# Performance work log

Hardware: AMD Instinct MI355X
Metric: run time of the kernel (lower is better)

Reference implementation:

```python
import jax, jax.numpy as jnp
import numpy as np


def setup_inputs() -> dict:
    key = jax.random.key(0)
    k_x, k_B, k_C, k_D, k_step = jax.random.split(key, 5)
    Bsz, L, H = 8, 4096, 512
    P = 256  # effective state dim = dim_ssm_state // 2 (conj_sym)
    # s4d_inv init for Lambda (complex, stored as real/imag parts)
    n = jnp.arange(P, dtype=jnp.float32)
    Lambda_re = -0.5 * jnp.ones((P,), dtype=jnp.float32)
    Lambda_im = (P / np.pi) * (P / (2.0 * n + 1.0) - 1.0)
    # lecun_normal-ish init for B (P,H,2) and C (H,P,2), divided by sqrt(2)
    B = jax.random.normal(k_B, (P, H, 2), dtype=jnp.float32) * (1.0 / np.sqrt(H)) / np.sqrt(2.0)
    C = jax.random.normal(k_C, (H, P, 2), dtype=jnp.float32) * (1.0 / np.sqrt(P)) / np.sqrt(2.0)
    D = jax.random.normal(k_D, (H,), dtype=jnp.float32)
    dt_min, dt_max = 1e-3, 1e-1
    log_step = jax.random.uniform(k_step, (P,)) * (np.log(dt_max) - np.log(dt_min)) + np.log(dt_min)
    x = jax.random.normal(k_x, (Bsz, L, H), dtype=jnp.float32)
    return {"x": x, "Lambda_re": Lambda_re, "Lambda_im": Lambda_im,
            "B": B, "C": C, "D": D, "log_step": log_step.astype(jnp.float32)}


def _binary_op(q_i, q_j):
    A_i, b_i = q_i
    A_j, b_j = q_j
    return (A_j * A_i, A_j * b_i + b_j)


def reference(x, Lambda_re, Lambda_im, B, C, D, log_step):
    # Assemble complex params (conj_sym=True)
    Lam = Lambda_re + 1j * Lambda_im          # (P,)
    B_tilde = B[..., 0] + 1j * B[..., 1]      # (P,H)
    C_tilde = C[..., 0] + 1j * C[..., 1]      # (H,P)
    step = jnp.exp(log_step)                  # (P,) step_rescale = 1.0
    # ZOH discretization
    Lambda_bar = jnp.exp(Lam * step)                              # (P,)
    B_bar = ((Lambda_bar - 1.0) / Lam)[:, None] * B_tilde         # (P,H)
    # Bu elements: (Bsz, L, P) complex
    Bu = jnp.einsum('blh,ph->blp', x.astype(B_bar.dtype), B_bar)
    Lam_elems = jnp.broadcast_to(Lambda_bar, Bu.shape)
    # Parallel linear recurrence over time axis
    _, xs = jax.lax.associative_scan(_binary_op, (Lam_elems, Bu), axis=1)
    # Output projection with conjugate symmetry + D skip
    ys = 2.0 * jnp.einsum('blp,hp->blh', xs, C_tilde).real + D * x
    return ys
```

## Files before the change

### kernel.cpp

```cpp
#include <hip/hip_runtime.h>
#include <hip/hip_bf16.h>
#include <hip/hip_fp16.h>
#include <math.h>

#define BSZ 8
#define LSEQ 4096
#define HDIM 512
#define PDIM 256
#define MROWS (BSZ * LSEQ)
#define NDIM 512
#define CHUNK 64
#define NCHUNK (LSEQ / CHUNK)

typedef __attribute__((ext_vector_type(8))) short bf16x8;
typedef __attribute__((ext_vector_type(4))) float f32x4;

__global__ __launch_bounds__(256) void convert_x(const float* __restrict__ x,
                                                 __hip_bfloat16* __restrict__ xb,
                                                 int n4) {
    int i = blockIdx.x * blockDim.x + threadIdx.x;
    if (i >= n4) return;
    float4 v = ((const float4*)x)[i];
    union { ushort4 u; __hip_bfloat16 h[4]; } o;
    o.h[0] = __float2bfloat16(v.x);
    o.h[1] = __float2bfloat16(v.y);
    o.h[2] = __float2bfloat16(v.z);
    o.h[3] = __float2bfloat16(v.w);
    ((ushort4*)xb)[i] = o.u;
}

__global__ void precompute_w1(const float* __restrict__ Lre,
                              const float* __restrict__ Lim,
                              const float* __restrict__ logstep,
                              const float* __restrict__ Bmat,
                              __hip_bfloat16* __restrict__ W1T,
                              float* __restrict__ a_re,
                              float* __restrict__ a_im) {
    int idx = blockIdx.x * blockDim.x + threadIdx.x;
    if (idx >= PDIM * HDIM) return;
    int p = idx / HDIM, h = idx % HDIM;
    double step = exp((double)logstep[p]);
    double dlr = (double)Lre[p], dli = (double)Lim[p];
    double mag = exp(dlr * step);
    double ar = mag * cos(dli * step);
    double ai = mag * sin(dli * step);
    double den = dlr * dlr + dli * dli;
    double nr = ar - 1.0, ni = ai;
    double fr = (nr * dlr + ni * dli) / den;
    double fi = (ni * dlr - nr * dli) / den;
    double br = (double)Bmat[(size_t)(p * HDIM + h) * 2 + 0];
    double bi = (double)Bmat[(size_t)(p * HDIM + h) * 2 + 1];
    W1T[(size_t)(2 * p) * HDIM + h]     = __float2bfloat16((float)(fr * br - fi * bi));
    W1T[(size_t)(2 * p + 1) * HDIM + h] = __float2bfloat16((float)(fr * bi + fi * br));
    if (h == 0) { a_re[p] = (float)ar; a_im[p] = (float)ai; }
}

__global__ void precompute_w2(const float* __restrict__ Cmat,
                              __hip_bfloat16* __restrict__ W2T) {
    int idx = blockIdx.x * blockDim.x + threadIdx.x;
    if (idx >= HDIM * PDIM) return;
    int h = idx / PDIM, p = idx % PDIM;
    float cr = Cmat[(size_t)(h * PDIM + p) * 2 + 0];
    float ci = Cmat[(size_t)(h * PDIM + p) * 2 + 1];
    W2T[(size_t)h * NDIM + 2 * p]     = __float2bfloat16(2.0f * cr);
    W2T[(size_t)h * NDIM + 2 * p + 1] = __float2bfloat16(-2.0f * ci);
}

template <typename OT, bool SKIP>
__global__ __launch_bounds__(256) void gemm_bt(
    const __hip_bfloat16* __restrict__ A,
    const __hip_bfloat16* __restrict__ BT,
    OT* __restrict__ C,
    const float* __restrict__ Dvec,
    const __hip_bfloat16* __restrict__ Xskip,
    int M, int N, int K) {
    __shared__ __hip_bfloat16 smA[128 * 32];
    __shared__ __hip_bfloat16 smB[128 * 32];

    const int tid = threadIdx.x;
    const int lane = tid & 63;
    const int wave = tid >> 6;
    const int row0 = blockIdx.x * 128;
    const int col0 = blockIdx.y * 128;
    const int wm = (wave >> 1) * 64;
    const int wn = (wave & 1) * 64;

    const int sr = lane >> 2;
    const int sk = (lane & 3) * 8;
    const int quad = lane >> 4;
    const int l15 = lane & 15;

    f32x4 acc[4][4] = {};

    for (int k0 = 0; k0 < K; k0 += 32) {
#pragma unroll
        for (int q = 0; q < 2; ++q) {
            const int chunk = wave * 32 + q * 16;
            const __hip_bfloat16* gA = A + (size_t)(row0 + chunk + sr) * K + k0 + sk;
            __builtin_amdgcn_global_load_lds(
                (const __attribute__((address_space(1))) void*)gA,
                (__attribute__((address_space(3))) void*)&smA[chunk * 32], 16, 0, 0);
            const __hip_bfloat16* gB = BT + (size_t)(col0 + chunk + sr) * K + k0 + sk;
            __builtin_amdgcn_global_load_lds(
                (const __attribute__((address_space(1))) void*)gB,
                (__attribute__((address_space(3))) void*)&smB[chunk * 32], 16, 0, 0);
        }
        __syncthreads();

        bf16x8 af[4], bfr[4];
#pragma unroll
        for (int i = 0; i < 4; ++i)
            af[i] = *(const bf16x8*)&smA[(wm + i * 16 + l15) * 32 + quad * 8];
#pragma unroll
        for (int j = 0; j < 4; ++j)
            bfr[j] = *(const bf16x8*)&smB[(wn + j * 16 + l15) * 32 + quad * 8];
#pragma unroll
        for (int i = 0; i < 4; ++i)
#pragma unroll
            for (int j = 0; j < 4; ++j)
                acc[i][j] = __builtin_amdgcn_mfma_f32_16x16x32_bf16(
                    af[i], bfr[j], acc[i][j], 0, 0, 0);
        __syncthreads();
    }

#pragma unroll
    for (int i = 0; i < 4; ++i) {
        const int mbase = row0 + wm + i * 16 + quad * 4;
#pragma unroll
        for (int j = 0; j < 4; ++j) {
            const int col = col0 + wn + j * 16 + l15;
            const float dv = SKIP ? Dvec[col] : 0.0f;
#pragma unroll
            for (int r = 0; r < 4; ++r) {
                const size_t m = (size_t)(mbase + r);
                float v = acc[i][j][r];
                if (SKIP) v += dv * __bfloat162float(Xskip[m * N + col]);
                if constexpr (sizeof(OT) == 2) {
                    C[m * N + col] = OT(v);
                } else {
                    C[m * N + col] = v;
                }
            }
        }
    }
}

__global__ __launch_bounds__(256) void scan_chunks(const __half2* __restrict__ Bu2,
                                                   const float* __restrict__ a_re,
                                                   const float* __restrict__ a_im,
                                                   float2* __restrict__ S) {
    int b = blockIdx.x / NCHUNK;
    int c = blockIdx.x % NCHUNK;
    int p = threadIdx.x;
    float ar = a_re[p], ai = a_im[p];
    float sr = 0.0f, si = 0.0f;
    size_t m0 = (size_t)b * LSEQ + (size_t)c * CHUNK;
    for (int j = 0; j < CHUNK; ++j) {
        float2 u = __half22float2(Bu2[(m0 + j) * PDIM + p]);
        float nsr = ar * sr - ai * si + u.x;
        float nsi = ar * si + ai * sr + u.y;
        sr = nsr; si = nsi;
    }
    S[(size_t)(b * NCHUNK + c) * PDIM + p] = make_float2(sr, si);
}

__global__ __launch_bounds__(256) void scan_carry(const float2* __restrict__ S,
                                                  const float* __restrict__ a_re,
                                                  const float* __restrict__ a_im,
                                                  float2* __restrict__ carry) {
    int b = blockIdx.x;
    int p = threadIdx.x;
    double ar = (double)a_re[p], ai = (double)a_im[p];
#pragma unroll
    for (int i = 0; i < 6; ++i) {
        double nr = ar * ar - ai * ai;
        double ni = 2.0 * ar * ai;
        ar = nr; ai = ni;
    }
    float alr = (float)ar, ali = (float)ai;
    float cr = 0.0f, ci = 0.0f;
    for (int c = 0; c < NCHUNK; ++c) {
        carry[(size_t)(b * NCHUNK + c) * PDIM + p] = make_float2(cr, ci);
        float2 s = S[(size_t)(b * NCHUNK + c) * PDIM + p];
        float ncr = alr * cr - ali * ci + s.x;
        float nci = alr * ci + ali * cr + s.y;
        cr = ncr; ci = nci;
    }
}

__global__ __launch_bounds__(256) void scan_apply(const __half2* __restrict__ Bu2,
                                                  const float* __restrict__ a_re,
                                                  const float* __restrict__ a_im,
                                                  const float2* __restrict__ carry,
                                                  ushort2* __restrict__ xsb2) {
    int b = blockIdx.x / NCHUNK;
    int c = blockIdx.x % NCHUNK;
    int p = threadIdx.x;
    float ar = a_re[p], ai = a_im[p];
    float2 c0 = carry[(size_t)(b * NCHUNK + c) * PDIM + p];
    float sr = c0.x, si = c0.y;
    size_t m0 = (size_t)b * LSEQ + (size_t)c * CHUNK;
    for (int j = 0; j < CHUNK; ++j) {
        size_t idx = (m0 + j) * PDIM + p;
        float2 u = __half22float2(Bu2[idx]);
        float nsr = ar * sr - ai * si + u.x;
        float nsi = ar * si + ai * sr + u.y;
        sr = nsr; si = nsi;
        union { ushort2 u2; __hip_bfloat16 h[2]; } o;
        o.h[0] = __float2bfloat16(sr);
        o.h[1] = __float2bfloat16(si);
        xsb2[idx] = o.u2;
    }
}

extern "C" void kernel_launch(void* const* d_in, const int* in_sizes, int n_in,
                              void* d_out, int out_size, void* d_ws, size_t ws_size,
                              hipStream_t stream) {
    const float* x       = (const float*)d_in[0];
    const float* Lre     = (const float*)d_in[1];
    const float* Lim     = (const float*)d_in[2];
    const float* Bmat    = (const float*)d_in[3];
    const float* Cmat    = (const float*)d_in[4];
    const float* Dvec    = (const float*)d_in[5];
    const float* logstep = (const float*)d_in[6];
    float* out = (float*)d_out;

    char* ws = (char*)d_ws;
    const size_t MB = 1u << 20;
    __hip_bfloat16* xb  = (__hip_bfloat16*)(ws + 0);
    __hip_bfloat16* xsb = (__hip_bfloat16*)(ws + 32 * MB);
    __half* Bu          = (__half*)(ws + 64 * MB);
    __hip_bfloat16* W1T = (__hip_bfloat16*)(ws + 96 * MB);
    __hip_bfloat16* W2T = (__hip_bfloat16*)(ws + 96 * MB + 512 * 1024);
    float*  a_re  = (float*)(ws + 97 * MB);
    float*  a_im  = (float*)(ws + 97 * MB + 4096);
    float2* S     = (float2*)(ws + 98 * MB);
    float2* carry = (float2*)(ws + 99 * MB);

    convert_x<<<(MROWS * HDIM / 4 + 255) / 256, 256, 0, stream>>>(
        x, xb, MROWS * HDIM / 4);
    precompute_w1<<<(PDIM * HDIM + 255) / 256, 256, 0, stream>>>(
        Lre, Lim, logstep, Bmat, W1T, a_re, a_im);
    precompute_w2<<<(HDIM * PDIM + 255) / 256, 256, 0, stream>>>(Cmat, W2T);

    dim3 ggrid(MROWS / 128, NDIM / 128);
    gemm_bt<__half, false><<<ggrid, 256, 0, stream>>>(
        xb, W1T, Bu, nullptr, nullptr, MROWS, NDIM, HDIM);

    scan_chunks<<<BSZ * NCHUNK, 256, 0, stream>>>((const __half2*)Bu, a_re, a_im, S);
    scan_carry<<<BSZ, 256, 0, stream>>>(S, a_re, a_im, carry);
    scan_apply<<<BSZ * NCHUNK, 256, 0, stream>>>((const __half2*)Bu, a_re, a_im,
                                                 carry, (ushort2*)xsb);

    dim3 ggrid2(MROWS / 128, HDIM / 128);
    gemm_bt<float, true><<<ggrid2, 256, 0, stream>>>(
        xsb, W2T, out, Dvec, xb, MROWS, HDIM, NDIM);
}
```

Baseline: 223.5 us.

## Double-buffer GEMM LDS, parallelize carry scan, hoist per-state discretization

The GEMM now keeps two LDS buffers and issues the next k-tile's global-to-LDS loads before computing the current tile, with one barrier per iteration, so load latency can overlap the MFMA work. The serial 64-step carry scan (8 blocks) becomes a wave-level Hillis-Steele shuffle scan across chunks, with one wave per (batch, state). The double-precision discretization, including the chunk-power of Lambda_bar, moves into a small one-block kernel so W1 construction runs in float instead of repeating the double math per element. These changes cost twice the LDS per GEMM block, which may lower occupancy, plus an extra kernel launch, and the shuffle scan may round slightly differently.

```diff
diff --git a/kernel.cpp b/kernel.cpp
--- a/kernel.cpp
+++ b/kernel.cpp
@@ -29,16 +29,14 @@
     ((ushort4*)xb)[i] = o.u;
 }
 
-__global__ void precompute_w1(const float* __restrict__ Lre,
-                              const float* __restrict__ Lim,
-                              const float* __restrict__ logstep,
-                              const float* __restrict__ Bmat,
-                              __hip_bfloat16* __restrict__ W1T,
-                              float* __restrict__ a_re,
-                              float* __restrict__ a_im) {
-    int idx = blockIdx.x * blockDim.x + threadIdx.x;
-    if (idx >= PDIM * HDIM) return;
-    int p = idx / HDIM, h = idx % HDIM;
+__global__ void precompute_params(const float* __restrict__ Lre,
+                                  const float* __restrict__ Lim,
+                                  const float* __restrict__ logstep,
+                                  float* __restrict__ f_re, float* __restrict__ f_im,
+                                  float* __restrict__ a_re, float* __restrict__ a_im,
+                                  float* __restrict__ al_re, float* __restrict__ al_im) {
+    int p = threadIdx.x;
+    if (p >= PDIM) return;
     double step = exp((double)logstep[p]);
     double dlr = (double)Lre[p], dli = (double)Lim[p];
     double mag = exp(dlr * step);
@@ -46,13 +44,33 @@
     double ai = mag * sin(dli * step);
     double den = dlr * dlr + dli * dli;
     double nr = ar - 1.0, ni = ai;
-    double fr = (nr * dlr + ni * dli) / den;
-    double fi = (ni * dlr - nr * dli) / den;
-    double br = (double)Bmat[(size_t)(p * HDIM + h) * 2 + 0];
-    double bi = (double)Bmat[(size_t)(p * HDIM + h) * 2 + 1];
-    W1T[(size_t)(2 * p) * HDIM + h]     = __float2bfloat16((float)(fr * br - fi * bi));
-    W1T[(size_t)(2 * p + 1) * HDIM + h] = __float2bfloat16((float)(fr * bi + fi * br));
-    if (h == 0) { a_re[p] = (float)ar; a_im[p] = (float)ai; }
+    f_re[p] = (float)((nr * dlr + ni * dli) / den);
+    f_im[p] = (float)((ni * dlr - nr * dli) / den);
+    a_re[p] = (float)ar;
+    a_im[p] = (float)ai;
+    double cr = ar, ci = ai;
+#pragma unroll
+    for (int i = 0; i < 6; ++i) {
+        double tr = cr * cr - ci * ci;
+        double ti = 2.0 * cr * ci;
+        cr = tr; ci = ti;
+    }
+    al_re[p] = (float)cr;
+    al_im[p] = (float)ci;
+}
+
+__global__ __launch_bounds__(256) void precompute_w1(
+    const float* __restrict__ f_re, const float* __restrict__ f_im,
+    const float* __restrict__ Bmat,
+    __hip_bfloat16* __restrict__ W1T) {
+    int idx = blockIdx.x * blockDim.x + threadIdx.x;
+    if (idx >= PDIM * HDIM) return;
+    int p = idx / HDIM, h = idx % HDIM;
+    float fr = f_re[p], fi = f_im[p];
+    float br = Bmat[(size_t)(p * HDIM + h) * 2 + 0];
+    float bi = Bmat[(size_t)(p * HDIM + h) * 2 + 1];
+    W1T[(size_t)(2 * p) * HDIM + h]     = __float2bfloat16(fr * br - fi * bi);
+    W1T[(size_t)(2 * p + 1) * HDIM + h] = __float2bfloat16(fr * bi + fi * br);
 }
 
 __global__ void precompute_w2(const float* __restrict__ Cmat,
@@ -74,8 +92,8 @@
     const float* __restrict__ Dvec,
     const __hip_bfloat16* __restrict__ Xskip,
     int M, int N, int K) {
-    __shared__ __hip_bfloat16 smA[128 * 32];
-    __shared__ __hip_bfloat16 smB[128 * 32];
+    __shared__ __hip_bfloat16 smA[2 * 128 * 32];
+    __shared__ __hip_bfloat16 smB[2 * 128 * 32];
 
     const int tid = threadIdx.x;
     const int lane = tid & 63;
@@ -92,35 +110,48 @@
 
     f32x4 acc[4][4] = {};
 
-    for (int k0 = 0; k0 < K; k0 += 32) {
+    auto stage = [&](int buf, int k0) {
 #pragma unroll
         for (int q = 0; q < 2; ++q) {
             const int chunk = wave * 32 + q * 16;
             const __hip_bfloat16* gA = A + (size_t)(row0 + chunk + sr) * K + k0 + sk;
             __builtin_amdgcn_global_load_lds(
                 (const __attribute__((address_space(1))) void*)gA,
-                (__attribute__((address_space(3))) void*)&smA[chunk * 32], 16, 0, 0);
+                (__attribute__((address_space(3))) void*)&smA[buf * 4096 + chunk * 32],
+                16, 0, 0);
             const __hip_bfloat16* gB = BT + (size_t)(col0 + chunk + sr) * K + k0 + sk;
             __builtin_amdgcn_global_load_lds(
                 (const __attribute__((address_space(1))) void*)gB,
-                (__attribute__((address_space(3))) void*)&smB[chunk * 32], 16, 0, 0);
+                (__attribute__((address_space(3))) void*)&smB[buf * 4096 + chunk * 32],
+                16, 0, 0);
         }
-        __syncthreads();
-
+    };
+
+    const int nk = K >> 5;
+    stage(0, 0);
+    __syncthreads();
+    int cur = 0;
+    for (int t = 0; t < nk; ++t) {
+        if (t + 1 < nk) stage(cur ^ 1, (t + 1) << 5);
+
+        const __hip_bfloat16* sA = &smA[cur * 4096];
+        const __hip_bfloat16* sB = &smB[cur * 4096];
         bf16x8 af[4], bfr[4];
 #pragma unroll
         for (int i = 0; i < 4; ++i)
-            af[i] = *(const bf16x8*)&smA[(wm + i * 16 + l15) * 32 + quad * 8];
+            af[i] = *(const bf16x8*)&sA[(wm + i * 16 + l15) * 32 + quad * 8];
 #pragma unroll
         for (int j = 0; j < 4; ++j)
-            bfr[j] = *(const bf16x8*)&smB[(wn + j * 16 + l15) * 32 + quad * 8];
+            bfr[j] = *(const bf16x8*)&sB[(wn + j * 16 + l15) * 32 + quad * 8];
 #pragma unroll
         for (int i = 0; i < 4; ++i)
 #pragma unroll
             for (int j = 0; j < 4; ++j)
                 acc[i][j] = __builtin_amdgcn_mfma_f32_16x16x32_bf16(
                     af[i], bfr[j], acc[i][j], 0, 0, 0);
+
         __syncthreads();
+        cur ^= 1;
     }
 
 #pragma unroll
@@ -165,27 +196,34 @@
 }
 
 __global__ __launch_bounds__(256) void scan_carry(const float2* __restrict__ S,
-                                                  const float* __restrict__ a_re,
-                                                  const float* __restrict__ a_im,
+                                                  const float* __restrict__ al_re,
+                                                  const float* __restrict__ al_im,
                                                   float2* __restrict__ carry) {
-    int b = blockIdx.x;
-    int p = threadIdx.x;
-    double ar = (double)a_re[p], ai = (double)a_im[p];
-#pragma unroll
-    for (int i = 0; i < 6; ++i) {
-        double nr = ar * ar - ai * ai;
-        double ni = 2.0 * ar * ai;
-        ar = nr; ai = ni;
-    }
-    float alr = (float)ar, ali = (float)ai;
-    float cr = 0.0f, ci = 0.0f;
-    for (int c = 0; c < NCHUNK; ++c) {
-        carry[(size_t)(b * NCHUNK + c) * PDIM + p] = make_float2(cr, ci);
-        float2 s = S[(size_t)(b * NCHUNK + c) * PDIM + p];
-        float ncr = alr * cr - ali * ci + s.x;
-        float nci = alr * ci + ali * cr + s.y;
-        cr = ncr; ci = nci;
-    }
+    const int wid = blockIdx.x * 4 + (threadIdx.x >> 6);
+    const int b = wid >> 8;
+    const int p = wid & 255;
+    const int c = threadIdx.x & 63;
+    float Ar = al_re[p], Ai = al_im[p];
+    float2 s = S[(size_t)(b * NCHUNK + c) * PDIM + p];
+    float br = s.x, bi = s.y;
+#pragma unroll
+    for (int d = 1; d < 64; d <<= 1) {
+        float pAr = __shfl_up(Ar, d);
+        float pAi = __shfl_up(Ai, d);
+        float pbr = __shfl_up(br, d);
+        float pbi = __shfl_up(bi, d);
+        if (c >= d) {
+            float nAr = Ar * pAr - Ai * pAi;
+            float nAi = Ar * pAi + Ai * pAr;
+            float nbr = Ar * pbr - Ai * pbi + br;
+            float nbi = Ar * pbi + Ai * pbr + bi;
+            Ar = nAr; Ai = nAi; br = nbr; bi = nbi;
+        }
+    }
+    float er = __shfl_up(br, 1);
+    float ei = __shfl_up(bi, 1);
+    if (c == 0) { er = 0.0f; ei = 0.0f; }
+    carry[(size_t)(b * NCHUNK + c) * PDIM + p] = make_float2(er, ei);
 }
 
 __global__ __launch_bounds__(256) void scan_apply(const __half2* __restrict__ Bu2,
@@ -234,13 +272,19 @@
     __hip_bfloat16* W2T = (__hip_bfloat16*)(ws + 96 * MB + 512 * 1024);
     float*  a_re  = (float*)(ws + 97 * MB);
     float*  a_im  = (float*)(ws + 97 * MB + 4096);
+    float*  f_re  = (float*)(ws + 97 * MB + 8192);
+    float*  f_im  = (float*)(ws + 97 * MB + 12288);
+    float*  al_re = (float*)(ws + 97 * MB + 16384);
+    float*  al_im = (float*)(ws + 97 * MB + 20480);
     float2* S     = (float2*)(ws + 98 * MB);
     float2* carry = (float2*)(ws + 99 * MB);
 
     convert_x<<<(MROWS * HDIM / 4 + 255) / 256, 256, 0, stream>>>(
         x, xb, MROWS * HDIM / 4);
+    precompute_params<<<1, 256, 0, stream>>>(Lre, Lim, logstep,
+                                             f_re, f_im, a_re, a_im, al_re, al_im);
     precompute_w1<<<(PDIM * HDIM + 255) / 256, 256, 0, stream>>>(
-        Lre, Lim, logstep, Bmat, W1T, a_re, a_im);
+        f_re, f_im, Bmat, W1T);
     precompute_w2<<<(HDIM * PDIM + 255) / 256, 256, 0, stream>>>(Cmat, W2T);
 
     dim3 ggrid(MROWS / 128, NDIM / 128);
@@ -248,7 +292,7 @@
         xb, W1T, Bu, nullptr, nullptr, MROWS, NDIM, HDIM);
 
     scan_chunks<<<BSZ * NCHUNK, 256, 0, stream>>>((const __half2*)Bu, a_re, a_im, S);
-    scan_carry<<<BSZ, 256, 0, stream>>>(S, a_re, a_im, carry);
+    scan_carry<<<BSZ * PDIM / 4, 256, 0, stream>>>(S, al_re, al_im, carry);
     scan_apply<<<BSZ * NCHUNK, 256, 0, stream>>>((const __half2*)Bu, a_re, a_im,
                                                  carry, (ushort2*)xsb);
 
```

After: 219.7 us. About the same (-1.7%).
